# Performance work log

Measured on AMD Instinct MI355X. Metric: run time of the kernel, lower is better.

## Reference

```python
import jax, jax.numpy as jnp
import numpy as np

GROUPS = 8
EPS = 1e-5


def setup_inputs() -> dict:
    key = jax.random.key(0)
    k1, k2, k3 = jax.random.split(key, 3)
    B, C, H, W = 4, 256, 64, 64
    x = jax.random.normal(k1, (B, C, H, W), dtype=jnp.float32)
    gamma = jnp.ones((C,), dtype=jnp.float32)
    beta = jnp.zeros((C,), dtype=jnp.float32)
    # conv1x1 weights flattened to [out, in]
    w_qkv = jax.random.normal(k2, (3 * C, C), dtype=jnp.float32) * (C ** -0.5)
    w_proj = jax.random.normal(k3, (C, C), dtype=jnp.float32) * (C ** -0.5)
    b_proj = jnp.zeros((C,), dtype=jnp.float32)
    return {"x": x, "gamma": gamma, "beta": beta, "w_qkv": w_qkv,
            "w_proj": w_proj, "b_proj": b_proj}


def group_norm(x, gamma, beta):
    B, C, H, W = x.shape
    xr = x.reshape(B, GROUPS, C // GROUPS, H * W)
    mu = xr.mean(axis=(2, 3), keepdims=True)
    var = xr.var(axis=(2, 3), keepdims=True)
    xn = (xr - mu) * jax.lax.rsqrt(var + EPS)
    xn = xn.reshape(B, C, H * W)
    return xn * gamma[None, :, None] + beta[None, :, None]


def reference(x, gamma, beta, w_qkv, w_proj, b_proj):
    B, C, H, W = x.shape
    N = H * W
    xn = group_norm(x, gamma, beta)               # [B, C, N]
    qkv = jnp.einsum('oc,bcn->bon', w_qkv, xn)    # [B, 3C, N]
    q, k, v = jnp.split(qkv, 3, axis=1)           # each [B, C, N]
    # attn[b, n, m] = sum_c q[b,c,n] * k[b,c,m] * C^-0.5
    scores = jnp.einsum('bcn,bcm->bnm', q, k) * (C ** -0.5)  # [B, N, N]
    attn = jax.nn.softmax(scores, axis=-1)
    # out = v @ attn^T  -> out[b,c,n] = sum_m v[b,c,m] * attn[b,n,m]
    out = jnp.einsum('bcm,bnm->bcn', v, attn)     # [B, C, N]
    y = jnp.einsum('oc,bcn->bon', w_proj, out) + b_proj[None, :, None]
    return x + y.reshape(B, C, H, W)
```

## Files before the change

### kernel.cpp

```cpp
#include <hip/hip_runtime.h>
#include <hip/hip_bf16.h>

#define BB 4
#define CC 256
#define NN 4096
#define GG 8
#define SPLITS 4
#define TKV 64
#define ITERS (NN / SPLITS / TKV)

typedef unsigned char u8;
typedef unsigned short u16;
typedef unsigned int u32;
typedef __bf16 b16x8 __attribute__((ext_vector_type(8)));
typedef float f32x4 __attribute__((ext_vector_type(4)));
typedef u32 u32x4 __attribute__((ext_vector_type(4)));
typedef u32 u32x2 __attribute__((ext_vector_type(2)));
typedef u16 u16x4 __attribute__((ext_vector_type(4)));

#define QS 0.09016844005556021f
#define FMAX 8.0f


__device__ __forceinline__ u16 f2bf(float f) {
    u32 u = __builtin_bit_cast(u32, f);
    u = (u + 0x7FFFu + ((u >> 16) & 1u)) >> 16;
    return (u16)u;
}

__device__ __forceinline__ float bf2f(u16 h) {
    return __builtin_bit_cast(float, (u32)h << 16);
}

__device__ __forceinline__ u32 pack_bf2(float a, float b) {
    float2 f; f.x = a; f.y = b;
    __hip_bfloat162 h = __float22bfloat162_rn(f);
    u32 r;
    __builtin_memcpy(&r, &h, 4);
    return r;
}

__device__ __forceinline__ float exp2_raw(float x) {
#if __has_builtin(__builtin_amdgcn_exp2f)
    return __builtin_amdgcn_exp2f(x);
#else
    float r;
    asm("v_exp_f32 %0, %1" : "=v"(r) : "v"(x));
    return r;
#endif
}

__device__ __forceinline__ b16x8 ldfrag(const u16* p) {
    u32x4 v = *reinterpret_cast<const u32x4*>(p);
    return __builtin_bit_cast(b16x8, v);
}

__device__ __forceinline__ int pk_fp8x4(float a, float b, float c, float d) {
    int r = __builtin_amdgcn_cvt_pk_fp8_f32(a, b, 0, false);
    r = __builtin_amdgcn_cvt_pk_fp8_f32(c, d, r, true);
    return r;
}

__device__ __forceinline__ long as_long(u32x2 v) { return __builtin_bit_cast(long, v); }

__device__ __forceinline__ u32 swz16(u32 v) {
    return (u32)__builtin_amdgcn_ds_swizzle((int)v, 0x401F);
}

__device__ __forceinline__ void pls32(u32& a, u32& b) {
    asm("v_permlane32_swap_b32 %0, %1" : "+v"(a), "+v"(b));
}

typedef __attribute__((address_space(1))) const unsigned int* gas_p;
typedef __attribute__((address_space(3))) unsigned int* las_p;

__device__ __forceinline__ void g2l(const u8* g, u8* l) {
    __builtin_amdgcn_global_load_lds((gas_p)g, (las_p)l, 16, 0, 0);
}

__device__ __forceinline__ void g2l16(const u16* g, u16* l) {
    __builtin_amdgcn_global_load_lds((gas_p)g, (las_p)l, 16, 0, 0);
}

__global__ void fold_w(const float* __restrict__ w_qkv, const float* __restrict__ w_proj,
                       const float* __restrict__ gamma, const float* __restrict__ beta,
                       const float* __restrict__ gsum,
                       u16* __restrict__ wqf, float* __restrict__ biasq,
                       u16* __restrict__ wpf) {
    int o = blockIdx.x;
    int b = blockIdx.y;
    int c = threadIdx.x;
    int g = c >> 5;
    const float inv = 1.f / ((CC / GG) * NN);
    float s  = gsum[(b * GG + g) * 2];
    float ss = gsum[(b * GG + g) * 2 + 1];
    float mu = s * inv;
    float rstd = rsqrtf(ss * inv - mu * mu + 1e-5f);
    float a  = gamma[c] * rstd;
    float bb = beta[c] - mu * a;
    float w = w_qkv[o * CC + c];
    size_t fe = ((size_t)((o >> 4) * 8 + (c >> 5)) * 64 + ((c & 31) >> 3) * 16 + (o & 15)) * 8 + (c & 7);
    wqf[(size_t)b * 768 * CC + fe] = f2bf(w * a);
    float part = w * bb;
    #pragma unroll
    for (int off = 32; off; off >>= 1) part += __shfl_down(part, off, 64);
    __shared__ float red[4];
    if ((threadIdx.x & 63) == 0) red[threadIdx.x >> 6] = part;
    __syncthreads();
    if (threadIdx.x == 0) biasq[b * 768 + o] = red[0] + red[1] + red[2] + red[3];
    if (b == 0 && o < CC) {
        float wp = w_proj[o * CC + c];
        wpf[fe] = f2bf(wp);
    }
}

__global__ void transpose_x(const float* __restrict__ x, u16* __restrict__ xtf,
                            float* __restrict__ gsum) {
    __shared__ float tile[64][65];
    __shared__ float red[4][4];
    int n0 = blockIdx.x * 64, c0 = blockIdx.y * 64, b = blockIdx.z;
    int t = threadIdx.x;
    int c4 = (t & 15) * 4;
    int r0 = t >> 4;
    const float* xp = x + (size_t)b * CC * NN;
    float s0 = 0.f, ss0 = 0.f, s1 = 0.f, ss1 = 0.f;
    #pragma unroll
    for (int i = 0; i < 4; ++i) {
        int row = i * 16 + r0;
        float4 v = *reinterpret_cast<const float4*>(&xp[(size_t)(c0 + row) * NN + n0 + c4]);
        tile[row][c4 + 0] = v.x; tile[row][c4 + 1] = v.y;
        tile[row][c4 + 2] = v.z; tile[row][c4 + 3] = v.w;
        float s = v.x + v.y + v.z + v.w;
        float q = v.x * v.x + v.y * v.y + v.z * v.z + v.w * v.w;
        if (i < 2) { s0 += s; ss0 += q; } else { s1 += s; ss1 += q; }
    }
    #pragma unroll
    for (int off = 32; off; off >>= 1) {
        s0 += __shfl_down(s0, off, 64); ss0 += __shfl_down(ss0, off, 64);
        s1 += __shfl_down(s1, off, 64); ss1 += __shfl_down(ss1, off, 64);
    }
    int wid = t >> 6;
    if ((t & 63) == 0) { red[wid][0] = s0; red[wid][1] = ss0; red[wid][2] = s1; red[wid][3] = ss1; }
    __syncthreads();
    if (t < 2) {
        float s  = red[0][t * 2] + red[1][t * 2] + red[2][t * 2] + red[3][t * 2];
        float ss = red[0][t * 2 + 1] + red[1][t * 2 + 1] + red[2][t * 2 + 1] + red[3][t * 2 + 1];
        int g = (c0 >> 5) + t;
        atomicAdd(&gsum[(b * GG + g) * 2], s);
        atomicAdd(&gsum[(b * GG + g) * 2 + 1], ss);
    }
    int nl = t >> 2;
    int cbq = t & 3;
    int l15 = nl & 15;
    int ntile = (n0 >> 4) + (nl >> 4);
    int kk = (c0 >> 5) + (cbq >> 1);
    u16* ob = xtf + (size_t)b * NN * CC;
    #pragma unroll
    for (int g = 0; g < 4; ++g) {
        int quad = (cbq & 1) * 2 + (g >> 1);
        int j0 = (g & 1) * 4;
        u16x4 v;
        v.x = f2bf(tile[cbq * 16 + g * 4 + 0][nl]);
        v.y = f2bf(tile[cbq * 16 + g * 4 + 1][nl]);
        v.z = f2bf(tile[cbq * 16 + g * 4 + 2][nl]);
        v.w = f2bf(tile[cbq * 16 + g * 4 + 3][nl]);
        *reinterpret_cast<u16x4*>(ob + ((size_t)(ntile * 8 + kk) * 64 + quad * 16 + l15) * 8 + j0) = v;
    }
}

__global__ void __launch_bounds__(256) qkv_gemm(const u16* __restrict__ wqf,
                                                const float* __restrict__ biasq,
                                                const u16* __restrict__ xtf,
                                                u8* __restrict__ qtf, u8* __restrict__ ktf,
                                                u8* __restrict__ vvf) {
    __shared__ u16 bx[16384];
    int b = blockIdx.z;
    int o0 = blockIdx.y * 128;
    int n0 = blockIdx.x * 64;
    int lane = threadIdx.x & 63, w = threadIdx.x >> 6;
    int l15 = lane & 15, quad = lane >> 4;
    const u16* Bg = xtf + (size_t)b * NN * CC + (size_t)n0 * 256;
    #pragma unroll
    for (int j = 0; j < 8; ++j) {
        int c = w * 8 + j;
        g2l16(Bg + (size_t)c * 512 + lane * 8, bx + (size_t)c * 512 + lane * 8);
    }
    __syncthreads();

    const u16* A = wqf + (size_t)b * 768 * CC;
    f32x4 acc[2][4] = {};
    #pragma unroll
    for (int kk = 0; kk < 8; ++kk) {
        b16x8 af[2];
        #pragma unroll
        for (int t = 0; t < 2; ++t) {
            int otile = (o0 >> 4) + w * 2 + t;
            af[t] = ldfrag(A + (size_t)(otile * 8 + kk) * 512 + lane * 8);
        }
        #pragma unroll
        for (int nt = 0; nt < 4; ++nt) {
            b16x8 bf = ldfrag(bx + (size_t)(nt * 8 + kk) * 512 + lane * 8);
            acc[0][nt] = __builtin_amdgcn_mfma_f32_16x16x32_bf16(af[0], bf, acc[0][nt], 0, 0, 0);
            acc[1][nt] = __builtin_amdgcn_mfma_f32_16x16x32_bf16(af[1], bf, acc[1][nt], 0, 0, 0);
        }
    }
    #pragma unroll
    for (int t = 0; t < 2; ++t) {
        int o_base = o0 + (w * 2 + t) * 16 + quad * 4;
        float bias[4];
        #pragma unroll
        for (int r = 0; r < 4; ++r) bias[r] = biasq[b * 768 + o_base + r];
        if (o0 < 512) {
            int oloc = (o0 < 256) ? o_base : (o_base - 256);
            u8* dst = ((o0 < 256) ? qtf : ktf) + (size_t)b * NN * CC;
            #pragma unroll
            for (int nt = 0; nt < 4; ++nt) {
                int n = n0 + nt * 16 + l15;
                int pk = pk_fp8x4(acc[t][nt][0] + bias[0], acc[t][nt][1] + bias[1],
                                  acc[t][nt][2] + bias[2], acc[t][nt][3] + bias[3]);
                size_t addr = (size_t)((n >> 4) * 4 + (oloc >> 6)) * 1024
                            + ((oloc & 31) >> 3) * 256 + (n & 15) * 16
                            + ((oloc >> 5) & 1) * 8 + (oloc & 7);
                *reinterpret_cast<u32*>(dst + addr) = (u32)pk;
            }
        } else {
            int cb = o_base - 512;
            u8* dst = vvf + (size_t)b * NN * CC;
            #pragma unroll
            for (int nt = 0; nt < 4; ++nt) {
                int kv = n0 + nt * 16 + l15;
                int pk = pk_fp8x4(acc[t][nt][0] + bias[0], acc[t][nt][1] + bias[1],
                                  acc[t][nt][2] + bias[2], acc[t][nt][3] + bias[3]);
                size_t base = (size_t)((kv >> 5) * 8 + (cb >> 5)) * 1024
                            + ((kv & 31) >> 3) * 256 + ((cb >> 4) & 1) * 8 + (kv & 7);
                #pragma unroll
                for (int r = 0; r < 4; ++r)
                    dst[base + ((cb & 15) + r) * 16] = (u8)(pk >> (r * 8));
            }
        }
    }
}

__global__ void __launch_bounds__(512, 4) flash(const u8* __restrict__ qtf,
                                                const u8* __restrict__ ktf,
                                                const u8* __restrict__ vvf,
                                                u16* __restrict__ po,
                                                float* __restrict__ lp) {
    __shared__ u8 kbuf[2][16384];
    __shared__ u8 vbuf[2][16384];
    int lin = blockIdx.x;
    int chunk = lin & 15;
    int nblk = lin >> 4;
    int b = chunk >> 2, sp = chunk & 3;
    int lane = threadIdx.x & 63, w = threadIdx.x >> 6;
    int l15 = lane & 15, quad = lane >> 4;
    int ntile = nblk * 8 + w;
    const u8* kb8 = ktf + (size_t)b * NN * CC;
    const u8* vb8 = vvf + (size_t)b * NN * CC;
    const bool qodd = (quad & 1) != 0;

    u32x4 aq[4];
    const u8* qb = qtf + (size_t)b * NN * CC + (size_t)ntile * 4096;
    #pragma unroll
    for (int s = 0; s < 4; ++s)
        aq[s] = *reinterpret_cast<const u32x4*>(qb + s * 1024 + lane * 16);

    f32x4 acco[16] = {};
    f32x4 accs[4] = {};
    float lsum = 0.f;

    const int m_beg = sp * (NN / SPLITS);

    auto stage_k = [&](int buf, int m0) {
        const u8* ks = kb8 + ((size_t)m0 << 8);
        #pragma unroll
        for (int j = 0; j < 2; ++j) {
            int idx = w * 2 + j;
            g2l(ks + idx * 1024 + lane * 16, &kbuf[buf][idx * 1024]);
        }
    };
    auto stage_v = [&](int buf, int m0) {
        const u8* vs = vb8 + ((size_t)m0 << 8);
        #pragma unroll
        for (int j = 0; j < 2; ++j) {
            int idx = w * 2 + j;
            g2l(vs + idx * 1024 + lane * 16, &vbuf[buf][idx * 1024]);
        }
    };
    auto qk_tile = [&](const u8* kc) {
        __builtin_amdgcn_s_setprio(1);
        #pragma unroll
        for (int s = 0; s < 4; ++s) {
            long qlo = as_long(u32x2{aq[s].x, aq[s].y});
            long qhi = as_long(u32x2{aq[s].z, aq[s].w});
            #pragma unroll
            for (int m = 0; m < 4; ++m) {
                u32x4 kf = *reinterpret_cast<const u32x4*>(kc + (size_t)(m * 4 + s) * 1024 + lane * 16);
                accs[m] = __builtin_amdgcn_mfma_f32_16x16x32_fp8_fp8(
                    as_long(u32x2{kf.x, kf.y}), qlo, accs[m], 0, 0, 0);
                accs[m] = __builtin_amdgcn_mfma_f32_16x16x32_fp8_fp8(
                    as_long(u32x2{kf.z, kf.w}), qhi, accs[m], 0, 0, 0);
            }
        }
        __builtin_amdgcn_s_setprio(0);
    };

    stage_k(0, m_beg);
    stage_v(0, m_beg);
    stage_k(1, m_beg + TKV);
    __syncthreads();
    qk_tile(&kbuf[0][0]);
    __syncthreads();

    for (int it = 0; it < ITERS; ++it) {
        int cur = it & 1;
        int pk[4];
        #pragma unroll
        for (int m = 0; m < 4; ++m) {
            float e0 = exp2_raw(fmaf(accs[m][0], QS, -FMAX));
            float e1 = exp2_raw(fmaf(accs[m][1], QS, -FMAX));
            float e2 = exp2_raw(fmaf(accs[m][2], QS, -FMAX));
            float e3 = exp2_raw(fmaf(accs[m][3], QS, -FMAX));
            lsum += (e0 + e1) + (e2 + e3);
            pk[m] = pk_fp8x4(e0, e1, e2, e3);
        }
        if (it + 1 < ITERS) {
            #pragma unroll
            for (int m = 0; m < 4; ++m) accs[m] = f32x4{0.f, 0.f, 0.f, 0.f};
            qk_tile(&kbuf[cur ^ 1][0]);
        }
        if (it + 2 < ITERS) stage_k(cur, m_beg + (it + 2) * TKV);
        if (it + 1 < ITERS) stage_v(cur ^ 1, m_beg + (it + 1) * TKV);
        const u8* vc = &vbuf[cur][0];
        #pragma unroll
        for (int h = 0; h < 2; ++h) {
            u32 a = (u32)pk[2 * h], bmat = (u32)pk[2 * h + 1];
            u32 ax = swz16(a), bx = swz16(bmat);
            pls32(a, bmat);
            pls32(ax, bx);
            u32 blo = qodd ? bx : a;
            u32 bhi = qodd ? bmat : ax;
            long bop = as_long(u32x2{blo, bhi});
            __builtin_amdgcn_s_setprio(1);
            #pragma unroll
            for (int c2 = 0; c2 < 8; ++c2) {
                u32x4 vf = *reinterpret_cast<const u32x4*>(vc + (size_t)(h * 8 + c2) * 1024 + lane * 16);
                acco[c2 * 2]     = __builtin_amdgcn_mfma_f32_16x16x32_fp8_fp8(
                    as_long(u32x2{vf.x, vf.y}), bop, acco[c2 * 2], 0, 0, 0);
                acco[c2 * 2 + 1] = __builtin_amdgcn_mfma_f32_16x16x32_fp8_fp8(
                    as_long(u32x2{vf.z, vf.w}), bop, acco[c2 * 2 + 1], 0, 0, 0);
            }
            __builtin_amdgcn_s_setprio(0);
        }
        __syncthreads();
    }
    u16* pochunk = po + ((size_t)(sp * BB + b) * 256 + ntile) * 4096;
    #pragma unroll
    for (int ct = 0; ct < 16; ++ct) {
        u32x2 st;
        st.x = pack_bf2(acco[ct][0], acco[ct][1]);
        st.y = pack_bf2(acco[ct][2], acco[ct][3]);
        *reinterpret_cast<u32x2*>(pochunk + (size_t)(ct * 64 + quad * 16 + l15) * 4) = st;
    }
    lsum += __shfl_xor(lsum, 16, 64);
    lsum += __shfl_xor(lsum, 32, 64);
    if (lane < 16)
        lp[(size_t)(sp * BB + b) * NN + ntile * 16 + l15] = lsum;
}

__global__ void __launch_bounds__(512) proj(const u16* __restrict__ wpf,
                                            const float* __restrict__ b_proj,
                                            const u16* __restrict__ po,
                                            const float* __restrict__ lp,
                                            const float* __restrict__ x,
                                            float* __restrict__ out) {
    __shared__ u16 bO[16384];
    int b = blockIdx.y, n0 = blockIdx.x * 64;
    int t = threadIdx.x;
    {
        int u = t & 127, ntl = t >> 7;
        int nb = (n0 >> 4) + ntl;
        int a = u & 7;
        int cblk = u >> 3;
        float accn[2][16] = {};
        float lsum2[2] = {};
        #pragma unroll
        for (int s = 0; s < SPLITS; ++s) {
            const u16* src = po + (((size_t)(s * BB + b) * 256 + nb) * 4096)
                           + cblk * 256 + a * 8;
            #pragma unroll
            for (int q4 = 0; q4 < 4; ++q4) {
                u16 s16[8];
                *reinterpret_cast<u32x4*>(s16) = *reinterpret_cast<const u32x4*>(src + q4 * 64);
                #pragma unroll
                for (int k = 0; k < 8; ++k)
                    accn[k >> 2][q4 * 4 + (k & 3)] += bf2f(s16[k]);
            }
            lsum2[0] += lp[(size_t)(s * BB + b) * NN + nb * 16 + a * 2];
            lsum2[1] += lp[(size_t)(s * BB + b) * NN + nb * 16 + a * 2 + 1];
        }
        #pragma unroll
        for (int nsel = 0; nsel < 2; ++nsel) {
            float inv = 1.f / lsum2[nsel];
            int row = a * 2 + nsel;
            #pragma unroll
            for (int h = 0; h < 2; ++h) {
                u16 outv[8];
                #pragma unroll
                for (int j = 0; j < 8; ++j) outv[j] = f2bf(accn[nsel][h * 8 + j] * inv);
                int kk = cblk >> 1, quad_f = (cblk & 1) * 2 + h;
                size_t off = ((size_t)(ntl * 8 + kk) * 64 + quad_f * 16 + row) * 8;
                *reinterpret_cast<u32x4*>(bO + off) = *reinterpret_cast<const u32x4*>(outv);
            }
        }
    }
    __syncthreads();
    int lane = t & 63, w = t >> 6;
    int l15 = lane & 15, quad = lane >> 4;
    f32x4 acc2[2][4] = {};
    #pragma unroll
    for (int kk = 0; kk < 8; ++kk) {
        b16x8 af[2];
        #pragma unroll
        for (int tt = 0; tt < 2; ++tt) {
            int otile = w * 2 + tt;
            af[tt] = ldfrag(wpf + (size_t)(otile * 8 + kk) * 512 + lane * 8);
        }
        #pragma unroll
        for (int nt = 0; nt < 4; ++nt) {
            b16x8 bf = ldfrag(bO + (size_t)(nt * 8 + kk) * 512 + lane * 8);
            acc2[0][nt] = __builtin_amdgcn_mfma_f32_16x16x32_bf16(af[0], bf, acc2[0][nt], 0, 0, 0);
            acc2[1][nt] = __builtin_amdgcn_mfma_f32_16x16x32_bf16(af[1], bf, acc2[1][nt], 0, 0, 0);
        }
    }
    #pragma unroll
    for (int tt = 0; tt < 2; ++tt) {
        int o_base = (w * 2 + tt) * 16 + quad * 4;
        #pragma unroll
        for (int nt = 0; nt < 4; ++nt) {
            int n = n0 + nt * 16 + l15;
            #pragma unroll
            for (int r = 0; r < 4; ++r) {
                int o = o_base + r;
                size_t idx = ((size_t)(b * CC + o)) * NN + n;
                out[idx] = acc2[tt][nt][r] + b_proj[o] + x[idx];
            }
        }
    }
}

extern "C" void kernel_launch(void* const* d_in, const int* in_sizes, int n_in,
                              void* d_out, int out_size, void* d_ws, size_t ws_size,
                              hipStream_t stream) {
    const float* x      = (const float*)d_in[0];
    const float* gamma  = (const float*)d_in[1];
    const float* beta   = (const float*)d_in[2];
    const float* w_qkv  = (const float*)d_in[3];
    const float* w_proj = (const float*)d_in[4];
    const float* b_proj = (const float*)d_in[5];
    float* out = (float*)d_out;

    char* p = (char*)d_ws;
    float* gsum  = (float*)p; p += 256;
    float* biasq = (float*)p; p += (size_t)BB * 768 * sizeof(float);
    u16* wqf = (u16*)p; p += (size_t)BB * 768 * CC * 2;
    u16* wpf = (u16*)p; p += (size_t)CC * CC * 2;
    u16* xtf = (u16*)p; p += (size_t)BB * NN * CC * 2;
    u8* qtf8 = (u8*)p; p += (size_t)BB * NN * CC;
    u8* ktf8 = (u8*)p; p += (size_t)BB * NN * CC;
    u8* vvf8 = (u8*)p; p += (size_t)BB * NN * CC;
    u16* po = (u16*)p; p += (size_t)SPLITS * BB * NN * CC * 2;
    float* lp = (float*)p; p += (size_t)SPLITS * BB * NN * sizeof(float);
    (void)ws_size; (void)in_sizes; (void)n_in; (void)out_size;

    (void)hipMemsetAsync(gsum, 0, BB * GG * 2 * sizeof(float), stream);
    transpose_x<<<dim3(NN / 64, CC / 64, BB), 256, 0, stream>>>(x, xtf, gsum);
    fold_w<<<dim3(768, BB), 256, 0, stream>>>(w_qkv, w_proj, gamma, beta, gsum, wqf, biasq, wpf);
    qkv_gemm<<<dim3(NN / 64, 6, BB), 256, 0, stream>>>(wqf, biasq, xtf, qtf8, ktf8, vvf8);
    flash<<<(NN / 128) * SPLITS * BB, 512, 0, stream>>>(qtf8, ktf8, vvf8, po, lp);
    proj<<<dim3(NN / 64, BB), 512, 0, stream>>>(wpf, b_proj, po, lp, x, out);
}
```

Measured before the change: 171.6 us.

## Process two query tiles per wave in flash kernel to reuse K/V fragments

```diff
diff --git a/kernel.cpp b/kernel.cpp
--- a/kernel.cpp
+++ b/kernel.cpp
@@ -241,7 +241,7 @@
     }
 }
 
-__global__ void __launch_bounds__(512, 4) flash(const u8* __restrict__ qtf,
+__global__ void __launch_bounds__(512, 2) flash(const u8* __restrict__ qtf,
                                                 const u8* __restrict__ ktf,
                                                 const u8* __restrict__ vvf,
                                                 u16* __restrict__ po,
@@ -254,20 +254,23 @@
     int b = chunk >> 2, sp = chunk & 3;
     int lane = threadIdx.x & 63, w = threadIdx.x >> 6;
     int l15 = lane & 15, quad = lane >> 4;
-    int ntile = nblk * 8 + w;
+    int ntile0 = nblk * 16 + w * 2;
     const u8* kb8 = ktf + (size_t)b * NN * CC;
     const u8* vb8 = vvf + (size_t)b * NN * CC;
     const bool qodd = (quad & 1) != 0;
 
-    u32x4 aq[4];
-    const u8* qb = qtf + (size_t)b * NN * CC + (size_t)ntile * 4096;
-    #pragma unroll
-    for (int s = 0; s < 4; ++s)
-        aq[s] = *reinterpret_cast<const u32x4*>(qb + s * 1024 + lane * 16);
-
-    f32x4 acco[16] = {};
-    f32x4 accs[4] = {};
-    float lsum = 0.f;
+    u32x4 aq[2][4];
+    const u8* qb = qtf + (size_t)b * NN * CC;
+    #pragma unroll
+    for (int t = 0; t < 2; ++t)
+        #pragma unroll
+        for (int s = 0; s < 4; ++s)
+            aq[t][s] = *reinterpret_cast<const u32x4*>(
+                qb + (size_t)(ntile0 + t) * 4096 + s * 1024 + lane * 16);
+
+    f32x4 acco[2][16] = {};
+    f32x4 accs[2][4] = {};
+    float lsum0 = 0.f, lsum1 = 0.f;
 
     const int m_beg = sp * (NN / SPLITS);
 
@@ -291,18 +294,31 @@
         __builtin_amdgcn_s_setprio(1);
         #pragma unroll
         for (int s = 0; s < 4; ++s) {
-            long qlo = as_long(u32x2{aq[s].x, aq[s].y});
-            long qhi = as_long(u32x2{aq[s].z, aq[s].w});
+            long q0lo = as_long(u32x2{aq[0][s].x, aq[0][s].y});
+            long q0hi = as_long(u32x2{aq[0][s].z, aq[0][s].w});
+            long q1lo = as_long(u32x2{aq[1][s].x, aq[1][s].y});
+            long q1hi = as_long(u32x2{aq[1][s].z, aq[1][s].w});
             #pragma unroll
             for (int m = 0; m < 4; ++m) {
                 u32x4 kf = *reinterpret_cast<const u32x4*>(kc + (size_t)(m * 4 + s) * 1024 + lane * 16);
-                accs[m] = __builtin_amdgcn_mfma_f32_16x16x32_fp8_fp8(
-                    as_long(u32x2{kf.x, kf.y}), qlo, accs[m], 0, 0, 0);
-                accs[m] = __builtin_amdgcn_mfma_f32_16x16x32_fp8_fp8(
-                    as_long(u32x2{kf.z, kf.w}), qhi, accs[m], 0, 0, 0);
+                long klo = as_long(u32x2{kf.x, kf.y});
+                long khi = as_long(u32x2{kf.z, kf.w});
+                accs[0][m] = __builtin_amdgcn_mfma_f32_16x16x32_fp8_fp8(klo, q0lo, accs[0][m], 0, 0, 0);
+                accs[0][m] = __builtin_amdgcn_mfma_f32_16x16x32_fp8_fp8(khi, q0hi, accs[0][m], 0, 0, 0);
+                accs[1][m] = __builtin_amdgcn_mfma_f32_16x16x32_fp8_fp8(klo, q1lo, accs[1][m], 0, 0, 0);
+                accs[1][m] = __builtin_amdgcn_mfma_f32_16x16x32_fp8_fp8(khi, q1hi, accs[1][m], 0, 0, 0);
             }
         }
         __builtin_amdgcn_s_setprio(0);
+    };
+    auto exch = [&](int pa, int pb) -> long {
+        u32 a = (u32)pa, bm = (u32)pb;
+        u32 ax = swz16(a), bx = swz16(bm);
+        pls32(a, bm);
+        pls32(ax, bx);
+        u32 blo = qodd ? bx : a;
+        u32 bhi = qodd ? bm : ax;
+        return as_long(u32x2{blo, bhi});
     };
 
     stage_k(0, m_beg);
@@ -314,19 +330,25 @@
 
     for (int it = 0; it < ITERS; ++it) {
         int cur = it & 1;
-        int pk[4];
-        #pragma unroll
-        for (int m = 0; m < 4; ++m) {
-            float e0 = exp2_raw(fmaf(accs[m][0], QS, -FMAX));
-            float e1 = exp2_raw(fmaf(accs[m][1], QS, -FMAX));
-            float e2 = exp2_raw(fmaf(accs[m][2], QS, -FMAX));
-            float e3 = exp2_raw(fmaf(accs[m][3], QS, -FMAX));
-            lsum += (e0 + e1) + (e2 + e3);
-            pk[m] = pk_fp8x4(e0, e1, e2, e3);
+        int pk[2][4];
+        #pragma unroll
+        for (int t = 0; t < 2; ++t) {
+            #pragma unroll
+            for (int m = 0; m < 4; ++m) {
+                float e0 = exp2_raw(fmaf(accs[t][m][0], QS, -FMAX));
+                float e1 = exp2_raw(fmaf(accs[t][m][1], QS, -FMAX));
+                float e2 = exp2_raw(fmaf(accs[t][m][2], QS, -FMAX));
+                float e3 = exp2_raw(fmaf(accs[t][m][3], QS, -FMAX));
+                if (t == 0) lsum0 += (e0 + e1) + (e2 + e3);
+                else        lsum1 += (e0 + e1) + (e2 + e3);
+                pk[t][m] = pk_fp8x4(e0, e1, e2, e3);
+            }
         }
         if (it + 1 < ITERS) {
             #pragma unroll
-            for (int m = 0; m < 4; ++m) accs[m] = f32x4{0.f, 0.f, 0.f, 0.f};
+            for (int t = 0; t < 2; ++t)
+                #pragma unroll
+                for (int m = 0; m < 4; ++m) accs[t][m] = f32x4{0.f, 0.f, 0.f, 0.f};
             qk_tile(&kbuf[cur ^ 1][0]);
         }
         if (it + 2 < ITERS) stage_k(cur, m_beg + (it + 2) * TKV);
@@ -334,38 +356,43 @@
         const u8* vc = &vbuf[cur][0];
         #pragma unroll
         for (int h = 0; h < 2; ++h) {
-            u32 a = (u32)pk[2 * h], bmat = (u32)pk[2 * h + 1];
-            u32 ax = swz16(a), bx = swz16(bmat);
-            pls32(a, bmat);
-            pls32(ax, bx);
-            u32 blo = qodd ? bx : a;
-            u32 bhi = qodd ? bmat : ax;
-            long bop = as_long(u32x2{blo, bhi});
+            long bop0 = exch(pk[0][2 * h], pk[0][2 * h + 1]);
+            long bop1 = exch(pk[1][2 * h], pk[1][2 * h + 1]);
             __builtin_amdgcn_s_setprio(1);
             #pragma unroll
             for (int c2 = 0; c2 < 8; ++c2) {
                 u32x4 vf = *reinterpret_cast<const u32x4*>(vc + (size_t)(h * 8 + c2) * 1024 + lane * 16);
-                acco[c2 * 2]     = __builtin_amdgcn_mfma_f32_16x16x32_fp8_fp8(
-                    as_long(u32x2{vf.x, vf.y}), bop, acco[c2 * 2], 0, 0, 0);
-                acco[c2 * 2 + 1] = __builtin_amdgcn_mfma_f32_16x16x32_fp8_fp8(
-                    as_long(u32x2{vf.z, vf.w}), bop, acco[c2 * 2 + 1], 0, 0, 0);
+                long vlo = as_long(u32x2{vf.x, vf.y});
+                long vhi = as_long(u32x2{vf.z, vf.w});
+                acco[0][c2 * 2]     = __builtin_amdgcn_mfma_f32_16x16x32_fp8_fp8(vlo, bop0, acco[0][c2 * 2], 0, 0, 0);
+                acco[0][c2 * 2 + 1] = __builtin_amdgcn_mfma_f32_16x16x32_fp8_fp8(vhi, bop0, acco[0][c2 * 2 + 1], 0, 0, 0);
+                acco[1][c2 * 2]     = __builtin_amdgcn_mfma_f32_16x16x32_fp8_fp8(vlo, bop1, acco[1][c2 * 2], 0, 0, 0);
+                acco[1][c2 * 2 + 1] = __builtin_amdgcn_mfma_f32_16x16x32_fp8_fp8(vhi, bop1, acco[1][c2 * 2 + 1], 0, 0, 0);
             }
             __builtin_amdgcn_s_setprio(0);
         }
         __syncthreads();
     }
-    u16* pochunk = po + ((size_t)(sp * BB + b) * 256 + ntile) * 4096;
-    #pragma unroll
-    for (int ct = 0; ct < 16; ++ct) {
-        u32x2 st;
-        st.x = pack_bf2(acco[ct][0], acco[ct][1]);
-        st.y = pack_bf2(acco[ct][2], acco[ct][3]);
-        *reinterpret_cast<u32x2*>(pochunk + (size_t)(ct * 64 + quad * 16 + l15) * 4) = st;
-    }
-    lsum += __shfl_xor(lsum, 16, 64);
-    lsum += __shfl_xor(lsum, 32, 64);
-    if (lane < 16)
-        lp[(size_t)(sp * BB + b) * NN + ntile * 16 + l15] = lsum;
+    #pragma unroll
+    for (int t = 0; t < 2; ++t) {
+        u16* pochunk = po + ((size_t)(sp * BB + b) * 256 + ntile0 + t) * 4096;
+        #pragma unroll
+        for (int ct = 0; ct < 16; ++ct) {
+            u32x2 st;
+            st.x = pack_bf2(acco[t][ct][0], acco[t][ct][1]);
+            st.y = pack_bf2(acco[t][ct][2], acco[t][ct][3]);
+            *reinterpret_cast<u32x2*>(pochunk + (size_t)(ct * 64 + quad * 16 + l15) * 4) = st;
+        }
+    }
+    lsum0 += __shfl_xor(lsum0, 16, 64);
+    lsum0 += __shfl_xor(lsum0, 32, 64);
+    lsum1 += __shfl_xor(lsum1, 16, 64);
+    lsum1 += __shfl_xor(lsum1, 32, 64);
+    if (lane < 16) {
+        size_t lb = (size_t)(sp * BB + b) * NN;
+        lp[lb + (size_t)ntile0 * 16 + l15] = lsum0;
+        lp[lb + (size_t)(ntile0 + 1) * 16 + l15] = lsum1;
+    }
 }
 
 __global__ void __launch_bounds__(512) proj(const u16* __restrict__ wpf,
@@ -477,6 +504,6 @@
     transpose_x<<<dim3(NN / 64, CC / 64, BB), 256, 0, stream>>>(x, xtf, gsum);
     fold_w<<<dim3(768, BB), 256, 0, stream>>>(w_qkv, w_proj, gamma, beta, gsum, wqf, biasq, wpf);
     qkv_gemm<<<dim3(NN / 64, 6, BB), 256, 0, stream>>>(wqf, biasq, xtf, qtf8, ktf8, vvf8);
-    flash<<<(NN / 128) * SPLITS * BB, 512, 0, stream>>>(qtf8, ktf8, vvf8, po, lp);
+    flash<<<(NN / 256) * SPLITS * BB, 512, 0, stream>>>(qtf8, ktf8, vvf8, po, lp);
     proj<<<dim3(NN / 64, BB), 512, 0, stream>>>(wpf, b_proj, po, lp, x, out);
 }
```

Result: slower. 176.6 us (+2.9%).

## Split each query tile's KV block across two waves with LDS reduction

Applied to the files above, without the earlier changes.

```diff
diff --git a/kernel.cpp b/kernel.cpp
--- a/kernel.cpp
+++ b/kernel.cpp
@@ -248,13 +248,15 @@
                                                 float* __restrict__ lp) {
     __shared__ u8 kbuf[2][16384];
     __shared__ u8 vbuf[2][16384];
+    __shared__ float lred[4][16];
     int lin = blockIdx.x;
     int chunk = lin & 15;
     int nblk = lin >> 4;
     int b = chunk >> 2, sp = chunk & 3;
     int lane = threadIdx.x & 63, w = threadIdx.x >> 6;
+    int qt = w & 3, half = w >> 2;
     int l15 = lane & 15, quad = lane >> 4;
-    int ntile = nblk * 8 + w;
+    int ntile = nblk * 4 + qt;
     const u8* kb8 = ktf + (size_t)b * NN * CC;
     const u8* vb8 = vvf + (size_t)b * NN * CC;
     const bool qodd = (quad & 1) != 0;
@@ -266,7 +268,8 @@
         aq[s] = *reinterpret_cast<const u32x4*>(qb + s * 1024 + lane * 16);
 
     f32x4 acco[16] = {};
-    f32x4 accs[4] = {};
+    f32x4 accs[2];
+    const f32x4 zz = {0.f, 0.f, 0.f, 0.f};
     float lsum = 0.f;
 
     const int m_beg = sp * (NN / SPLITS);
@@ -294,15 +297,25 @@
             long qlo = as_long(u32x2{aq[s].x, aq[s].y});
             long qhi = as_long(u32x2{aq[s].z, aq[s].w});
             #pragma unroll
-            for (int m = 0; m < 4; ++m) {
+            for (int mm = 0; mm < 2; ++mm) {
+                int m = half * 2 + mm;
                 u32x4 kf = *reinterpret_cast<const u32x4*>(kc + (size_t)(m * 4 + s) * 1024 + lane * 16);
-                accs[m] = __builtin_amdgcn_mfma_f32_16x16x32_fp8_fp8(
-                    as_long(u32x2{kf.x, kf.y}), qlo, accs[m], 0, 0, 0);
-                accs[m] = __builtin_amdgcn_mfma_f32_16x16x32_fp8_fp8(
-                    as_long(u32x2{kf.z, kf.w}), qhi, accs[m], 0, 0, 0);
+                accs[mm] = __builtin_amdgcn_mfma_f32_16x16x32_fp8_fp8(
+                    as_long(u32x2{kf.x, kf.y}), qlo, (s == 0) ? zz : accs[mm], 0, 0, 0);
+                accs[mm] = __builtin_amdgcn_mfma_f32_16x16x32_fp8_fp8(
+                    as_long(u32x2{kf.z, kf.w}), qhi, accs[mm], 0, 0, 0);
             }
         }
         __builtin_amdgcn_s_setprio(0);
+    };
+    auto exch = [&](int pa, int pb) -> long {
+        u32 a = (u32)pa, bm = (u32)pb;
+        u32 ax = swz16(a), bx = swz16(bm);
+        pls32(a, bm);
+        pls32(ax, bx);
+        u32 blo = qodd ? bx : a;
+        u32 bhi = qodd ? bm : ax;
+        return as_long(u32x2{blo, bhi});
     };
 
     stage_k(0, m_beg);
@@ -314,58 +327,61 @@
 
     for (int it = 0; it < ITERS; ++it) {
         int cur = it & 1;
-        int pk[4];
-        #pragma unroll
-        for (int m = 0; m < 4; ++m) {
-            float e0 = exp2_raw(fmaf(accs[m][0], QS, -FMAX));
-            float e1 = exp2_raw(fmaf(accs[m][1], QS, -FMAX));
-            float e2 = exp2_raw(fmaf(accs[m][2], QS, -FMAX));
-            float e3 = exp2_raw(fmaf(accs[m][3], QS, -FMAX));
+        int pk[2];
+        #pragma unroll
+        for (int mm = 0; mm < 2; ++mm) {
+            float e0 = exp2_raw(fmaf(accs[mm][0], QS, -FMAX));
+            float e1 = exp2_raw(fmaf(accs[mm][1], QS, -FMAX));
+            float e2 = exp2_raw(fmaf(accs[mm][2], QS, -FMAX));
+            float e3 = exp2_raw(fmaf(accs[mm][3], QS, -FMAX));
             lsum += (e0 + e1) + (e2 + e3);
-            pk[m] = pk_fp8x4(e0, e1, e2, e3);
-        }
-        if (it + 1 < ITERS) {
-            #pragma unroll
-            for (int m = 0; m < 4; ++m) accs[m] = f32x4{0.f, 0.f, 0.f, 0.f};
-            qk_tile(&kbuf[cur ^ 1][0]);
-        }
+            pk[mm] = pk_fp8x4(e0, e1, e2, e3);
+        }
+        if (it + 1 < ITERS) qk_tile(&kbuf[cur ^ 1][0]);
         if (it + 2 < ITERS) stage_k(cur, m_beg + (it + 2) * TKV);
         if (it + 1 < ITERS) stage_v(cur ^ 1, m_beg + (it + 1) * TKV);
         const u8* vc = &vbuf[cur][0];
-        #pragma unroll
-        for (int h = 0; h < 2; ++h) {
-            u32 a = (u32)pk[2 * h], bmat = (u32)pk[2 * h + 1];
-            u32 ax = swz16(a), bx = swz16(bmat);
-            pls32(a, bmat);
-            pls32(ax, bx);
-            u32 blo = qodd ? bx : a;
-            u32 bhi = qodd ? bmat : ax;
-            long bop = as_long(u32x2{blo, bhi});
-            __builtin_amdgcn_s_setprio(1);
-            #pragma unroll
-            for (int c2 = 0; c2 < 8; ++c2) {
-                u32x4 vf = *reinterpret_cast<const u32x4*>(vc + (size_t)(h * 8 + c2) * 1024 + lane * 16);
-                acco[c2 * 2]     = __builtin_amdgcn_mfma_f32_16x16x32_fp8_fp8(
-                    as_long(u32x2{vf.x, vf.y}), bop, acco[c2 * 2], 0, 0, 0);
-                acco[c2 * 2 + 1] = __builtin_amdgcn_mfma_f32_16x16x32_fp8_fp8(
-                    as_long(u32x2{vf.z, vf.w}), bop, acco[c2 * 2 + 1], 0, 0, 0);
-            }
-            __builtin_amdgcn_s_setprio(0);
-        }
+        long bop = exch(pk[0], pk[1]);
+        __builtin_amdgcn_s_setprio(1);
+        #pragma unroll
+        for (int c2 = 0; c2 < 8; ++c2) {
+            u32x4 vf = *reinterpret_cast<const u32x4*>(vc + (size_t)(half * 8 + c2) * 1024 + lane * 16);
+            acco[c2 * 2]     = __builtin_amdgcn_mfma_f32_16x16x32_fp8_fp8(
+                as_long(u32x2{vf.x, vf.y}), bop, acco[c2 * 2], 0, 0, 0);
+            acco[c2 * 2 + 1] = __builtin_amdgcn_mfma_f32_16x16x32_fp8_fp8(
+                as_long(u32x2{vf.z, vf.w}), bop, acco[c2 * 2 + 1], 0, 0, 0);
+        }
+        __builtin_amdgcn_s_setprio(0);
         __syncthreads();
     }
-    u16* pochunk = po + ((size_t)(sp * BB + b) * 256 + ntile) * 4096;
-    #pragma unroll
-    for (int ct = 0; ct < 16; ++ct) {
-        u32x2 st;
-        st.x = pack_bf2(acco[ct][0], acco[ct][1]);
-        st.y = pack_bf2(acco[ct][2], acco[ct][3]);
-        *reinterpret_cast<u32x2*>(pochunk + (size_t)(ct * 64 + quad * 16 + l15) * 4) = st;
-    }
+
     lsum += __shfl_xor(lsum, 16, 64);
     lsum += __shfl_xor(lsum, 32, 64);
-    if (lane < 16)
-        lp[(size_t)(sp * BB + b) * NN + ntile * 16 + l15] = lsum;
+
+    u8* cb = (qt == 0) ? &kbuf[0][0] : (qt == 1) ? &kbuf[1][0]
+           : (qt == 2) ? &vbuf[0][0] : &vbuf[1][0];
+    if (half) {
+        #pragma unroll
+        for (int ct = 0; ct < 16; ++ct)
+            *reinterpret_cast<f32x4*>(cb + (size_t)ct * 1024 + lane * 16) = acco[ct];
+        if (lane < 16) lred[qt][l15] = lsum;
+    }
+    __syncthreads();
+    if (!half) {
+        #pragma unroll
+        for (int ct = 0; ct < 16; ++ct)
+            acco[ct] += *reinterpret_cast<const f32x4*>(cb + (size_t)ct * 1024 + lane * 16);
+        u16* pochunk = po + ((size_t)(sp * BB + b) * 256 + ntile) * 4096;
+        #pragma unroll
+        for (int ct = 0; ct < 16; ++ct) {
+            u32x2 st;
+            st.x = pack_bf2(acco[ct][0], acco[ct][1]);
+            st.y = pack_bf2(acco[ct][2], acco[ct][3]);
+            *reinterpret_cast<u32x2*>(pochunk + (size_t)(ct * 64 + quad * 16 + l15) * 4) = st;
+        }
+        if (lane < 16)
+            lp[(size_t)(sp * BB + b) * NN + ntile * 16 + l15] = lsum + lred[qt][l15];
+    }
 }
 
 __global__ void __launch_bounds__(512) proj(const u16* __restrict__ wpf,
@@ -477,6 +493,6 @@
     transpose_x<<<dim3(NN / 64, CC / 64, BB), 256, 0, stream>>>(x, xtf, gsum);
     fold_w<<<dim3(768, BB), 256, 0, stream>>>(w_qkv, w_proj, gamma, beta, gsum, wqf, biasq, wpf);
     qkv_gemm<<<dim3(NN / 64, 6, BB), 256, 0, stream>>>(wqf, biasq, xtf, qtf8, ktf8, vvf8);
-    flash<<<(NN / 128) * SPLITS * BB, 512, 0, stream>>>(qtf8, ktf8, vvf8, po, lp);
+    flash<<<(NN / 64) * SPLITS * BB, 512, 0, stream>>>(qtf8, ktf8, vvf8, po, lp);
     proj<<<dim3(NN / 64, BB), 512, 0, stream>>>(wpf, b_proj, po, lp, x, out);
 }
```

Measured after the change: 175.2 us. 1.02x slower.
